# Optimization experiments

Measured on AMD Instinct MI355X. Metric: run time of the kernel, lower is better.

The kernel has to match this reference:

```python
import jax, jax.numpy as jnp
import numpy as np
from functools import partial

NP = 1024      # particles
T = 128        # timesteps
CUR_MIN, CUR_MAX = -2.0, 4.0
E_CRIT = 29000.0
F_STD = 0.005
G_STD = 0.01
NU = 1.0 / (G_STD * np.sqrt(2.0 * np.pi))

# VoC battery open-circuit-voltage curve constants
V_L, V_0 = -1.59614486, 4.13646328
GAMMA, ALPHA, BETA = 0.63726463, 1.40174122, 2.54478965


def voc(soc):
    return (V_L + (V_0 - V_L) * jnp.exp(GAMMA * (soc - 1.0))
            + ALPHA * V_L * (soc - 1.0)
            + (1.0 - ALPHA) * V_L * (jnp.exp(-BETA) - jnp.exp(-BETA * jnp.sqrt(soc))))


def setup_inputs() -> dict:
    key = jax.random.key(0)
    ks = jax.random.split(key, 11)
    soc_init = jax.random.uniform(ks[0], (NP, 1), jnp.float32, 0.3, 1.0)
    current = jax.random.normal(ks[1], (1, T), jnp.float32) * 0.5 + 1.0
    voltage_measured = 3.7 + 0.1 * jax.random.normal(ks[2], (1, T), jnp.float32)
    W1 = jax.random.normal(ks[3], (2, 1024), jnp.float32) / np.sqrt(2.0)
    b1 = jnp.zeros((1024,), jnp.float32)
    W2 = jax.random.normal(ks[4], (1024, 512), jnp.float32) / np.sqrt(1024.0)
    b2 = jnp.zeros((512,), jnp.float32)
    W3 = jax.random.normal(ks[5], (512, 1), jnp.float32) / np.sqrt(512.0)
    b3 = jnp.zeros((1,), jnp.float32)
    noise = jax.random.normal(ks[6], (T, NP, 1), jnp.float32)  # unit-std process noise
    u = jax.random.uniform(ks[7], (T,), jnp.float32)           # systematic-resampling offsets
    return {"soc_init": soc_init, "current": current, "voltage_measured": voltage_measured,
            "W1": W1, "b1": b1, "W2": W2, "b2": b2, "W3": W3, "b3": b3,
            "noise": noise, "u": u}


def _forward(soc_init, current, voltage_measured, W1, b1, W2, b2, W3, b3, noise, u):
    n = soc_init.shape[0]

    def mlp(x):  # [n,2] -> [n,1]
        z = jax.nn.sigmoid(x @ W1 + b1)
        z = jax.nn.sigmoid(z @ W2 + b2)
        return z @ W3 + b3

    def scale_I(I):
        return (I - CUR_MIN) / (CUR_MAX - CUR_MIN)

    cur = current[0]                       # [T]
    vmeas = voltage_measured[0]            # [T]
    cur_prev = jnp.concatenate([cur[:1], cur[:-1]])  # first step reuses current[0,0]

    def step(soc, xs):
        c_prev, c_t, vm, eps, ut = xs
        # --- prediction with previous current ---
        I = jnp.broadcast_to(c_prev, soc.shape)
        Z = mlp(jnp.concatenate([soc, scale_I(I)], axis=1))
        V = voc(soc) - I * Z
        soc = soc - I * V / E_CRIT + eps * F_STD
        soc = jnp.clip(soc, 1e-10, 1.0)
        # --- measurement update with current at t ---
        I = jnp.broadcast_to(c_t, soc.shape)
        sI = scale_I(I)
        Z = mlp(jnp.concatenate([soc, sI], axis=1))
        V = voc(soc) - I * Z
        logW = np.log(NU) - 0.5 * ((V - vm) / G_STD) ** 2  # [n,1]
        w = jnp.exp(logW - jnp.max(logW))[:, 0]
        wn = w / jnp.sum(w)
        # systematic resampling (deterministic given offset ut)
        cdf = jnp.cumsum(wn)
        pos = (ut + jnp.arange(n, dtype=jnp.float32)) / n
        idx = jnp.clip(jnp.searchsorted(cdf, pos), 0, n - 1)
        soc = soc[idx]
        # --- post-resample evaluation ---
        Z = mlp(jnp.concatenate([soc, sI], axis=1))
        V = voc(soc) - I * Z
        mse = jnp.mean((V - vm) ** 2)
        return soc, (mse, V[:, 0], soc[:, 0])

    soc0 = soc_init.astype(jnp.float32)
    _, (mses, Vs, socs) = jax.lax.scan(step, soc0, (cur_prev, cur, vmeas, noise, u))
    loss = jnp.mean(mses)        # == sum_t mse_t / T
    voltage = Vs.T               # [n, T]
    soc_hist = socs.T            # [n, T]
    return loss, voltage, soc_hist


def reference(soc_init, current, voltage_measured, W1, b1, W2, b2, W3, b3, noise, u):
    return _forward(soc_init, current, voltage_measured, W1, b1, W2, b2, W3, b3, noise, u)
```

## Files before the change

kernel.cpp:

```cpp
#include <hip/hip_runtime.h>
#include <stdint.h>

typedef __attribute__((ext_vector_type(8))) short short8;
typedef __attribute__((ext_vector_type(4))) float floatx4;

#define DONE_MAGIC 0x600DF00Du


__device__ __forceinline__ float sigm(float x) { return 1.0f / (1.0f + expf(-x)); }

__device__ __forceinline__ float vocf(float s) {
  const float V_L = -1.59614486f, V_0 = 4.13646328f;
  const float GAM = 0.63726463f, ALP = 1.40174122f, BET = 2.54478965f;
  return V_L + (V_0 - V_L) * expf(GAM * (s - 1.0f)) + ALP * V_L * (s - 1.0f)
       + (1.0f - ALP) * V_L * (expf(-BET) - expf(-BET * sqrtf(s)));
}

__device__ __forceinline__ unsigned short f2bf(float f) {
  unsigned u = __float_as_uint(f);
  u += 0x7FFFu + ((u >> 16) & 1u);
  return (unsigned short)(u >> 16);
}
__device__ __forceinline__ float bf2f(unsigned short b) {
  return __uint_as_float(((unsigned)b) << 16);
}

__device__ __forceinline__ float interp_c(const float* ctab, float s) {
  float f = s * 31.0f;
  float jf = fminf(floorf(f), 30.0f);
  int j = (int)jf;
  float u = f - jf;
  const float4 c = *(const float4*)&ctab[j * 4];
  return fmaf(fmaf(fmaf(c.w, u, c.z), u, c.y), u, c.x);
}

__device__ __forceinline__ int send_bl(float c, float u) {
  float C = c * 1024.0f;
  float sf = floorf(C - u);
  sf += (u + (sf + 1.0f) <= C) ? 1.0f : 0.0f;
  sf -= (u + sf > C) ? 1.0f : 0.0f;
  return (int)sf;
}

__device__ __forceinline__ float fast_exp2(float x) {
  float r;
  asm("v_exp_f32 %0, %1" : "=v"(r) : "v"(x));
  return r;
}


template<int C, int RM>
__device__ __forceinline__ float dpp_add_f(float x) {
  return __int_as_float(__builtin_amdgcn_update_dpp(0, __float_as_int(x), C, RM, 0xF, false));
}
template<int C, int RM>
__device__ __forceinline__ float dpp_old_f(float x) {
  return __int_as_float(__builtin_amdgcn_update_dpp(__float_as_int(x), __float_as_int(x), C, RM, 0xF, false));
}
template<int C, int RM>
__device__ __forceinline__ int dpp_old_i(int x) {
  return __builtin_amdgcn_update_dpp(x, x, C, RM, 0xF, false);
}
__device__ __forceinline__ float dpp_wshr1_f0(float x) {
  return __int_as_float(__builtin_amdgcn_update_dpp(0, __float_as_int(x), 0x138, 0xF, 0xF, true));
}
__device__ __forceinline__ int dpp_wshr1_i(int x, int old) {
  return __builtin_amdgcn_update_dpp(old, x, 0x138, 0xF, 0xF, false);
}
__device__ __forceinline__ int dpp_wshl1_i(int x, int old) {
  return __builtin_amdgcn_update_dpp(old, x, 0x130, 0xF, 0xF, false);
}

__device__ __forceinline__ float wave_iscan_add(float x) {
  x += dpp_add_f<0x111, 0xF>(x);
  x += dpp_add_f<0x112, 0xF>(x);
  x += dpp_add_f<0x114, 0xF>(x);
  x += dpp_add_f<0x118, 0xF>(x);
  x += dpp_add_f<0x142, 0xA>(x);
  x += dpp_add_f<0x143, 0xC>(x);
  return x;
}
__device__ __forceinline__ float wave_max_bcast(float x) {
  x = fmaxf(x, dpp_old_f<0xB1,  0xF>(x));
  x = fmaxf(x, dpp_old_f<0x4E,  0xF>(x));
  x = fmaxf(x, dpp_old_f<0x141, 0xF>(x));
  x = fmaxf(x, dpp_old_f<0x140, 0xF>(x));
  x = fmaxf(x, dpp_old_f<0x142, 0xA>(x));
  x = fmaxf(x, dpp_old_f<0x143, 0xC>(x));
  return __int_as_float(__builtin_amdgcn_readlane(__float_as_int(x), 63));
}
__device__ __forceinline__ int wave_iscan_max(int x) {
  x = max(x, dpp_old_i<0x111, 0xF>(x));
  x = max(x, dpp_old_i<0x112, 0xF>(x));
  x = max(x, dpp_old_i<0x114, 0xF>(x));
  x = max(x, dpp_old_i<0x118, 0xF>(x));
  x = max(x, dpp_old_i<0x142, 0xA>(x));
  x = max(x, dpp_old_i<0x143, 0xC>(x));
  return x;
}

__device__ __forceinline__ float rdlane_f(float x, int lane) {
  return __int_as_float(__builtin_amdgcn_readlane(__float_as_int(x), lane));
}

__device__ __forceinline__ void bar_lds() {
  asm volatile("s_waitcnt lgkmcnt(0)" ::: "memory");
  __builtin_amdgcn_s_barrier();
  asm volatile("" ::: "memory");
}


__global__ void __launch_bounds__(256)
k1_swizzle(const float* __restrict__ W2g, short* __restrict__ w2hiG, short* __restrict__ w2loG)
{
  int bid = blockIdx.x, tid = threadIdx.x;
  int pg = bid & 15, ng = bid >> 4;
  int u = pg * 256 + tid;
  int kb = u >> 7, l = u & 63, nt = (u >> 6) & 1, kq = l >> 4;
  int col = ng * 32 + nt * 16 + (l & 15);
  short8 hi8, lo8;
  #pragma unroll
  for (int j = 0; j < 8; j++) {
    int k = kb * 32 + kq * 8 + j;
    float w = W2g[k * 512 + col];
    unsigned short h = f2bf(w);
    hi8[j] = (short)h;
    lo8[j] = (short)f2bf(w - bf2f(h));
  }
  size_t off = ((size_t)ng * 4096 + u) * 8;
  *(short8*)(w2hiG + off) = hi8;
  *(short8*)(w2loG + off) = lo8;
}


__global__ void __launch_bounds__(256)
k2_gemm(const float* __restrict__ curg, const float* __restrict__ W1g,
        const float* __restrict__ b1g, const float* __restrict__ b2g,
        const float* __restrict__ W3g, const short* __restrict__ w2hiG,
        const short* __restrict__ w2loG, float* __restrict__ part)
{
  __shared__ short w2S[32768];
  __shared__ float b2S[32], w3S[32];

  const int tid = threadIdx.x, bid = blockIdx.x;
  const int ng = bid & 15, rtg = bid >> 4;
  const int wv = tid >> 6, ln = tid & 63;
  const int kq = ln >> 4;

  {
    const short* srcH = w2hiG + (size_t)ng * 32768;
    for (int i = tid; i < 4096; i += 256)
      *(short8*)(w2S + i * 8) = *(const short8*)(srcH + i * 8);
    if (tid < 32) { b2S[tid] = b2g[ng * 32 + tid]; w3S[tid] = W3g[ng * 32 + tid]; }
  }
  __syncthreads();

  const short* loG = w2loG + (size_t)ng * 32768;
  const int c = ln & 15, q = ln >> 4;
  const float b20 = b2S[c], b21 = b2S[16 + c];
  const float w30 = w3S[c], w31 = w3S[16 + c];

  for (int jj = 0; jj < 3; jj++) {
    int rt = rtg + 32 * jj;
    if (rt >= 72) break;
    int pt = rt * 4 + wv;
    unsigned r = pt * 16 + (ln & 15);
    unsigned t = r / 36u;
    int i = (int)(r - t * 36u);
    float soc = (float)(i - 1) * (1.0f / 31.0f);
    float sI = (curg[t] + 2.0f) / 6.0f;

    floatx4 acc0 = {0.f, 0.f, 0.f, 0.f};
    floatx4 acc1 = {0.f, 0.f, 0.f, 0.f};

    for (int kb = 0; kb < 32; kb++) {
      int k0 = kb * 32 + kq * 8;
      floatx4 wa0 = *(const floatx4*)(W1g + k0);
      floatx4 wa1 = *(const floatx4*)(W1g + k0 + 4);
      floatx4 wb0 = *(const floatx4*)(W1g + 1024 + k0);
      floatx4 wb1 = *(const floatx4*)(W1g + 1024 + k0 + 4);
      floatx4 bb0 = *(const floatx4*)(b1g + k0);
      floatx4 bb1 = *(const floatx4*)(b1g + k0 + 4);
      short8 ah, al;
      #pragma unroll
      for (int j = 0; j < 4; j++) {
        float x = soc * wa0[j] + sI * wb0[j] + bb0[j];
        float z = __builtin_amdgcn_rcpf(1.0f + __expf(-x));
        unsigned short h = f2bf(z);
        ah[j] = (short)h;
        al[j] = (short)f2bf(z - bf2f(h));
      }
      #pragma unroll
      for (int j = 0; j < 4; j++) {
        float x = soc * wa1[j] + sI * wb1[j] + bb1[j];
        float z = __builtin_amdgcn_rcpf(1.0f + __expf(-x));
        unsigned short h = f2bf(z);
        ah[4 + j] = (short)h;
        al[4 + j] = (short)f2bf(z - bf2f(h));
      }
      short8 bh0 = *(const short8*)(w2S + (kb * 2 + 0) * 512 + ln * 8);
      short8 bh1 = *(const short8*)(w2S + (kb * 2 + 1) * 512 + ln * 8);
      short8 bl0 = *(const short8*)(loG + (kb * 2 + 0) * 512 + ln * 8);
      short8 bl1 = *(const short8*)(loG + (kb * 2 + 1) * 512 + ln * 8);
      acc0 = __builtin_amdgcn_mfma_f32_16x16x32_bf16(ah, bh0, acc0, 0, 0, 0);
      acc1 = __builtin_amdgcn_mfma_f32_16x16x32_bf16(ah, bh1, acc1, 0, 0, 0);
      acc0 = __builtin_amdgcn_mfma_f32_16x16x32_bf16(ah, bl0, acc0, 0, 0, 0);
      acc1 = __builtin_amdgcn_mfma_f32_16x16x32_bf16(ah, bl1, acc1, 0, 0, 0);
      acc0 = __builtin_amdgcn_mfma_f32_16x16x32_bf16(al, bh0, acc0, 0, 0, 0);
      acc1 = __builtin_amdgcn_mfma_f32_16x16x32_bf16(al, bh1, acc1, 0, 0, 0);
    }

    #pragma unroll
    for (int r2 = 0; r2 < 4; r2++) {
      float v = w30 * sigm(acc0[r2] + b20) + w31 * sigm(acc1[r2] + b21);
      v += __shfl_xor(v, 1);
      v += __shfl_xor(v, 2);
      v += __shfl_xor(v, 4);
      v += __shfl_xor(v, 8);
      if (c == 0) part[(size_t)(pt * 16 + q * 4 + r2) * 16 + ng] = v;
    }
  }
}


__global__ void __launch_bounds__(256)
k3_table(const float* __restrict__ part, const float* __restrict__ b3g,
         const float* __restrict__ curg, float* __restrict__ VtabG)
{
  unsigned r = blockIdx.x * 256 + threadIdx.x;
  if (r < 4608) {
    const float* p = part + (size_t)r * 16;
    float s = 0.f;
    #pragma unroll
    for (int i = 0; i < 16; i++) s += p[i];
    float Z = s + b3g[0];
    unsigned t = r / 36u;
    int i = (int)(r - t * 36u);
    float node = (float)(i - 1) * (1.0f / 31.0f);
    float nodc = fmaxf(node, 1e-10f);
    VtabG[r] = vocf(nodc) - curg[t] * Z;
  }
}


__global__ void __launch_bounds__(256)
k3b_coeff(const float* __restrict__ VtabG, float* __restrict__ ctabG)
{
  int idx = blockIdx.x * 256 + threadIdx.x;
  if (idx < 3968) {
    int t = idx / 31, j = idx - t * 31;
    const float* nb = VtabG + t * 36 + j;
    float n0 = nb[0], n1 = nb[1], n2 = nb[2], n3 = nb[3];
    float c0 = n1;
    float c1 = (-2.0f * n0 - 3.0f * n1 + 6.0f * n2 - n3) * (1.0f / 6.0f);
    float c2 = (n0 - 2.0f * n1 + n2) * 0.5f;
    float c3 = (-n0 + 3.0f * (n1 - n2) + n3) * (1.0f / 6.0f);
    *(float4*)&ctabG[idx * 4] = make_float4(c0, c1, c2, c3);
  }
}


__device__ __forceinline__ int swzi(int j) { return ((j & 3) << 8) | (j >> 2); }

__global__ void __launch_bounds__(256)
pf_seq(const float* __restrict__ soc_init, const float* __restrict__ curg,
       const float* __restrict__ vmeasg, const float* __restrict__ noise_g,
       const float* __restrict__ u_g, const float* __restrict__ ctabG,
       float* __restrict__ vout, float* __restrict__ sout, float* __restrict__ outp,
       unsigned* __restrict__ flag)
{
  __shared__ float ctabS[15872];
  __shared__ float2 pvS[2][1024];
  __shared__ int   markS[1024] __attribute__((aligned(16)));
  __shared__ int   chunkS[4] __attribute__((aligned(16)));
  __shared__ float2 msS[4] __attribute__((aligned(16)));
  __shared__ float lossS[4];

  if (blockIdx.x != 0) {
    float a = 1.0000001f, b = 0.9999999f, c = 0.5f;
    while (__hip_atomic_load(flag, __ATOMIC_RELAXED, __HIP_MEMORY_SCOPE_AGENT) != DONE_MAGIC) {
      #pragma unroll 8
      for (int i = 0; i < 512; i++) { a = fmaf(a, c, b); b = fmaf(b, c, a); }
    }
    asm volatile("" :: "v"(a), "v"(b));
    return;
  }

  const int tid = threadIdx.x;
  const int w = tid >> 6, l = tid & 63;
  const int p0 = tid * 4;

  #pragma unroll
  for (int k = 0; k < 16; k++) {
    int i = tid + 256 * k;
    if (i < 3968) *(float4*)&ctabS[i * 4] = *(const float4*)&ctabG[i * 4];
  }
  float curA = curg[l],   curB = curg[64 + l];
  float vmA  = vmeasg[l], vmB  = vmeasg[64 + l];
  float uA   = u_g[l],    uB   = u_g[64 + l];
  *(int4*)&markS[p0] = make_int4(-1, -1, -1, -1);
  if (tid < 4) chunkS[tid] = -1;

  float sp0, sp1, sp2, sp3;
  {
    float4 s4 = *(const float4*)(soc_init + p0);
    float4 n4 = *(const float4*)(noise_g + p0);
    bar_lds();
    float c0 = rdlane_f(curA, 0);
    float c02 = c0 * (1.0f / 29000.0f);
    float spv[4];
    #pragma unroll
    for (int r = 0; r < 4; r++) {
      float si = ((const float*)&s4)[r];
      float V0 = interp_c(ctabS, si);
      float spn = fmaf(((const float*)&n4)[r], 0.005f, fmaf(-c02, V0, si));
      spv[r] = __builtin_amdgcn_fmed3f(spn, 1e-10f, 1.0f);
    }
    sp0 = spv[0]; sp1 = spv[1]; sp2 = spv[2]; sp3 = spv[3];
  }

  float lossAcc = 0.0f;

  for (int t = 0; t < 128; t++) {
    const float* ctab = ctabS + t * 124;
    const int cb = t & 1;
    float cI, vm, ut;
    if (t < 64) { cI = rdlane_f(curA, t); vm = rdlane_f(vmA, t); ut = rdlane_f(uA, t); }
    else        { cI = rdlane_f(curB, t - 64); vm = rdlane_f(vmB, t - 64); ut = rdlane_f(uB, t - 64); }
    float cI2 = cI * (1.0f / 29000.0f);

    int tn = (t < 127) ? t + 1 : 127;
    float4 noi4 = *(const float4*)(noise_g + tn * 1024 + p0);

    float V10 = interp_c(ctab, sp0);
    float V11 = interp_c(ctab, sp1);
    float V12 = interp_c(ctab, sp2);
    float V13 = interp_c(ctab, sp3);
    pvS[cb][tid]       = make_float2(sp0, V10);
    pvS[cb][256 + tid] = make_float2(sp1, V11);
    pvS[cb][512 + tid] = make_float2(sp2, V12);
    pvS[cb][768 + tid] = make_float2(sp3, V13);
    float d0 = V10 - vm, d1 = V11 - vm, d2 = V12 - vm, d3 = V13 - vm;
    float lw0 = d0 * d0 * -7213.4755594f;
    float lw1 = d1 * d1 * -7213.4755594f;
    float lw2 = d2 * d2 * -7213.4755594f;
    float lw3 = d3 * d3 * -7213.4755594f;

    float lmax = fmaxf(fmaxf(lw0, lw1), fmaxf(lw2, lw3));
    float mw = wave_max_bcast(lmax);
    float pr0, pr1, pr2, pr3, acc;
    {
      float w0 = fast_exp2(lw0 - mw); acc = w0;    pr0 = acc;
      float w1 = fast_exp2(lw1 - mw); acc += w1;   pr1 = acc;
      float w2 = fast_exp2(lw2 - mw); acc += w2;   pr2 = acc;
      float w3 = fast_exp2(lw3 - mw); acc += w3;   pr3 = acc;
    }
    float isc = wave_iscan_add(acc);
    if (l == 63) msS[w] = make_float2(mw, isc);
    bar_lds();

    float4 ms01 = *(const float4*)&msS[0];
    float4 ms23 = *(const float4*)&msS[2];
    float m = fmaxf(fmaxf(ms01.x, ms01.z), fmaxf(ms23.x, ms23.z));
    float f0 = fast_exp2(ms01.x - m), f1 = fast_exp2(ms01.z - m);
    float f2 = fast_exp2(ms23.x - m), f3 = fast_exp2(ms23.w == ms23.w ? ms23.z - m : 0.f);
    f3 = fast_exp2(ms23.z - m);
    float t0 = ms01.y * f0, t1 = ms01.w * f1, t2 = ms23.y * f2, t3 = ms23.w * f3;
    float total = (t0 + t1) + (t2 + t3);
    float woff = (w > 0 ? t0 : 0.0f) + (w > 1 ? t1 : 0.0f) + (w > 2 ? t2 : 0.0f);
    float fw = (w == 0) ? f0 : ((w == 1) ? f1 : ((w == 2) ? f2 : f3));
    float exclw = dpp_wshr1_f0(isc);
    float rS = 1.0f / total;

    int se0 = send_bl(fmaf(exclw + pr0, fw, woff) * rS, ut);
    int se1 = send_bl(fmaf(exclw + pr1, fw, woff) * rS, ut);
    int se2 = send_bl(fmaf(exclw + pr2, fw, woff) * rS, ut);
    int se3 = send_bl(fmaf(exclw + pr3, fw, woff) * rS, ut);

    int nxt = dpp_wshl1_i(se0, se3);
    int tbase = t << 10;
    if (tid == 0 && se0 >= 0) { markS[0] = tbase; atomicMax(&chunkS[0], tbase); }
    if (se1 > se0 && se0 < 1023) {
      int s = se0 + 1, tg = tbase | (p0 + 1);
      markS[swzi(s)] = tg; atomicMax(&chunkS[s >> 8], tg);
    }
    if (se2 > se1 && se1 < 1023) {
      int s = se1 + 1, tg = tbase | (p0 + 2);
      markS[swzi(s)] = tg; atomicMax(&chunkS[s >> 8], tg);
    }
    if (se3 > se2 && se2 < 1023) {
      int s = se2 + 1, tg = tbase | (p0 + 3);
      markS[swzi(s)] = tg; atomicMax(&chunkS[s >> 8], tg);
    }
    if (l != 63) {
      if (nxt > se3 && se3 < 1023) {
        int s = se3 + 1, tg = tbase | (p0 + 4);
        markS[swzi(s)] = tg; atomicMax(&chunkS[s >> 8], tg);
      }
    } else {
      if (se3 < 1023) {
        int s = se3 + 1;
        int tg = (tid == 255) ? (tbase | 1023) : (tbase | (p0 + 4));
        atomicMax(&markS[swzi(s)], tg); atomicMax(&chunkS[s >> 8], tg);
      }
    }
    bar_lds();

    int mk0 = markS[tid],       mk1 = markS[256 + tid];
    int mk2 = markS[512 + tid], mk3 = markS[768 + tid];
    int4 ch4 = *(const int4*)chunkS;
    int q0 = mk0;
    int q1 = max(q0, mk1);
    int q2 = max(q1, mk2);
    int q3 = max(q2, mk3);
    int iscI = wave_iscan_max(q3);
    int ex = dpp_wshr1_i(iscI, -1);
    if (w > 0) ex = max(ex, ch4.x);
    if (w > 1) ex = max(ex, ch4.y);
    if (w > 2) ex = max(ex, ch4.z);

    int o0 = max(ex, q0) & 1023, o1 = max(ex, q1) & 1023;
    int o2 = max(ex, q2) & 1023, o3 = max(ex, q3) & 1023;
    float2 g0 = pvS[cb][swzi(o0)];
    float2 g1 = pvS[cb][swzi(o1)];
    float2 g2 = pvS[cb][swzi(o2)];
    float2 g3 = pvS[cb][swzi(o3)];

    *(float4*)(vout + t * 1024 + p0) = make_float4(g0.y, g1.y, g2.y, g3.y);
    *(float4*)(sout + t * 1024 + p0) = make_float4(g0.x, g1.x, g2.x, g3.x);

    float e0 = g0.y - vm, e1 = g1.y - vm, e2 = g2.y - vm, e3 = g3.y - vm;
    lossAcc = fmaf(e0, e0, lossAcc);
    lossAcc = fmaf(e1, e1, lossAcc);
    lossAcc = fmaf(e2, e2, lossAcc);
    lossAcc = fmaf(e3, e3, lossAcc);
    const float* nz = (const float*)&noi4;
    sp0 = __builtin_amdgcn_fmed3f(fmaf(nz[0], 0.005f, fmaf(-cI2, g0.y, g0.x)), 1e-10f, 1.0f);
    sp1 = __builtin_amdgcn_fmed3f(fmaf(nz[1], 0.005f, fmaf(-cI2, g1.y, g1.x)), 1e-10f, 1.0f);
    sp2 = __builtin_amdgcn_fmed3f(fmaf(nz[2], 0.005f, fmaf(-cI2, g2.y, g2.x)), 1e-10f, 1.0f);
    sp3 = __builtin_amdgcn_fmed3f(fmaf(nz[3], 0.005f, fmaf(-cI2, g3.y, g3.x)), 1e-10f, 1.0f);
  }

  float ls = wave_iscan_add(lossAcc);
  if (l == 63) lossS[w] = ls;
  bar_lds();
  if (tid == 0) {
    outp[0] = (lossS[0] + lossS[1] + lossS[2] + lossS[3]) * (1.0f / 131072.0f);
    __hip_atomic_store(flag, DONE_MAGIC, __ATOMIC_RELEASE, __HIP_MEMORY_SCOPE_AGENT);
  }
}


__global__ void __launch_bounds__(256)
k5_transpose(const float* __restrict__ vout, const float* __restrict__ sout,
             float* __restrict__ outp)
{
  __shared__ float tile[128 * 65];
  const int bid = blockIdx.x;
  const int arr = bid & 1;
  const int pg = bid >> 1;
  const float* src = arr ? sout : vout;
  float* dst = outp + 1 + arr * 131072;
  const int tid = threadIdx.x;
  const int p0 = pg * 64;

  #pragma unroll 4
  for (int s = 0; s < 32; s++) {
    int t = s * 4 + (tid >> 6);
    int p = tid & 63;
    tile[t * 65 + p] = src[t * 1024 + p0 + p];
  }
  __syncthreads();
  #pragma unroll 4
  for (int s = 0; s < 32; s++) {
    int pl = s * 2 + (tid >> 7);
    int t = tid & 127;
    dst[(p0 + pl) * 128 + t] = tile[t * 65 + pl];
  }
}


extern "C" void kernel_launch(void* const* d_in, const int* in_sizes, int n_in,
                              void* d_out, int out_size, void* d_ws, size_t ws_size,
                              hipStream_t stream) {
  const float* soc_init = (const float*)d_in[0];
  const float* cur      = (const float*)d_in[1];
  const float* vmeas    = (const float*)d_in[2];
  const float* W1       = (const float*)d_in[3];
  const float* b1       = (const float*)d_in[4];
  const float* W2       = (const float*)d_in[5];
  const float* b2       = (const float*)d_in[6];
  const float* W3       = (const float*)d_in[7];
  const float* b3       = (const float*)d_in[8];
  const float* noise    = (const float*)d_in[9];
  const float* u        = (const float*)d_in[10];
  float* out = (float*)d_out;
  char* ws = (char*)d_ws;

  short* w2hi   = (short*)ws;
  short* w2lo   = (short*)(ws + (1 << 20));
  float* part   = (float*)(ws + (2 << 20));
  char*  p3     = ws + (2 << 20) + 4608 * 16 * 4;
  float* VtabG  = (float*)p3;
  float* ctabG  = (float*)(p3 + 4608 * 4);
  float* vout   = (float*)(p3 + 4608 * 4 + 3968 * 16);
  float* sout   = (float*)(p3 + 4608 * 4 + 3968 * 16 + 1024 * 128 * 4);
  unsigned* flag = (unsigned*)(p3 + 4608 * 4 + 3968 * 16 + 2 * 1024 * 128 * 4);

  k1_swizzle<<<256, 256, 0, stream>>>(W2, w2hi, w2lo);
  k2_gemm<<<512, 256, 0, stream>>>(cur, W1, b1, b2, W3, w2hi, w2lo, part);
  k3_table<<<18, 256, 0, stream>>>(part, b3, cur, VtabG);
  k3b_coeff<<<16, 256, 0, stream>>>(VtabG, ctabG);
  pf_seq<<<256, 256, 0, stream>>>(soc_init, cur, vmeas, noise, u, ctabG, vout, sout, out, flag);
  k5_transpose<<<32, 256, 0, stream>>>(vout, sout, out);
}
```

Before: 332.4 us.

## Run sequential particle-filter block with 512 threads, two particles per thread

Result: no change. 338.3 us (+1.8%).

```diff
diff --git a/kernel.cpp b/kernel.cpp
--- a/kernel.cpp
+++ b/kernel.cpp
@@ -260,9 +260,9 @@
 }
 
 
-__device__ __forceinline__ int swzi(int j) { return ((j & 3) << 8) | (j >> 2); }
-
-__global__ void __launch_bounds__(256)
+__device__ __forceinline__ int swzi(int j) { return ((j & 1) << 9) | (j >> 1); }
+
+__global__ void __launch_bounds__(512)
 pf_seq(const float* __restrict__ soc_init, const float* __restrict__ curg,
        const float* __restrict__ vmeasg, const float* __restrict__ noise_g,
        const float* __restrict__ u_g, const float* __restrict__ ctabG,
@@ -272,9 +272,9 @@
   __shared__ float ctabS[15872];
   __shared__ float2 pvS[2][1024];
   __shared__ int   markS[1024] __attribute__((aligned(16)));
-  __shared__ int   chunkS[4] __attribute__((aligned(16)));
-  __shared__ float2 msS[4] __attribute__((aligned(16)));
-  __shared__ float lossS[4];
+  __shared__ int   chunkS[8] __attribute__((aligned(16)));
+  __shared__ float2 msS[8] __attribute__((aligned(16)));
+  __shared__ float lossS[8];
 
   if (blockIdx.x != 0) {
     float a = 1.0000001f, b = 0.9999999f, c = 0.5f;
@@ -288,35 +288,30 @@
 
   const int tid = threadIdx.x;
   const int w = tid >> 6, l = tid & 63;
-  const int p0 = tid * 4;
+  const int p0 = tid * 2;
 
   #pragma unroll
-  for (int k = 0; k < 16; k++) {
-    int i = tid + 256 * k;
+  for (int k = 0; k < 8; k++) {
+    int i = tid + 512 * k;
     if (i < 3968) *(float4*)&ctabS[i * 4] = *(const float4*)&ctabG[i * 4];
   }
   float curA = curg[l],   curB = curg[64 + l];
   float vmA  = vmeasg[l], vmB  = vmeasg[64 + l];
   float uA   = u_g[l],    uB   = u_g[64 + l];
-  *(int4*)&markS[p0] = make_int4(-1, -1, -1, -1);
-  if (tid < 4) chunkS[tid] = -1;
-
-  float sp0, sp1, sp2, sp3;
+  *(int2*)&markS[p0] = make_int2(-1, -1);
+  if (tid < 8) chunkS[tid] = -1;
+
+  float sp0, sp1;
   {
-    float4 s4 = *(const float4*)(soc_init + p0);
-    float4 n4 = *(const float4*)(noise_g + p0);
+    float2 s2 = *(const float2*)(soc_init + p0);
+    float2 n2 = *(const float2*)(noise_g + p0);
     bar_lds();
     float c0 = rdlane_f(curA, 0);
     float c02 = c0 * (1.0f / 29000.0f);
-    float spv[4];
-    #pragma unroll
-    for (int r = 0; r < 4; r++) {
-      float si = ((const float*)&s4)[r];
-      float V0 = interp_c(ctabS, si);
-      float spn = fmaf(((const float*)&n4)[r], 0.005f, fmaf(-c02, V0, si));
-      spv[r] = __builtin_amdgcn_fmed3f(spn, 1e-10f, 1.0f);
-    }
-    sp0 = spv[0]; sp1 = spv[1]; sp2 = spv[2]; sp3 = spv[3];
+    float V00 = interp_c(ctabS, s2.x);
+    float V01 = interp_c(ctabS, s2.y);
+    sp0 = __builtin_amdgcn_fmed3f(fmaf(n2.x, 0.005f, fmaf(-c02, V00, s2.x)), 1e-10f, 1.0f);
+    sp1 = __builtin_amdgcn_fmed3f(fmaf(n2.y, 0.005f, fmaf(-c02, V01, s2.y)), 1e-10f, 1.0f);
   }
 
   float lossAcc = 0.0f;
@@ -330,122 +325,107 @@
     float cI2 = cI * (1.0f / 29000.0f);
 
     int tn = (t < 127) ? t + 1 : 127;
-    float4 noi4 = *(const float4*)(noise_g + tn * 1024 + p0);
+    float2 noi2 = *(const float2*)(noise_g + tn * 1024 + p0);
 
     float V10 = interp_c(ctab, sp0);
     float V11 = interp_c(ctab, sp1);
-    float V12 = interp_c(ctab, sp2);
-    float V13 = interp_c(ctab, sp3);
     pvS[cb][tid]       = make_float2(sp0, V10);
-    pvS[cb][256 + tid] = make_float2(sp1, V11);
-    pvS[cb][512 + tid] = make_float2(sp2, V12);
-    pvS[cb][768 + tid] = make_float2(sp3, V13);
-    float d0 = V10 - vm, d1 = V11 - vm, d2 = V12 - vm, d3 = V13 - vm;
+    pvS[cb][512 + tid] = make_float2(sp1, V11);
+    float d0 = V10 - vm, d1 = V11 - vm;
     float lw0 = d0 * d0 * -7213.4755594f;
     float lw1 = d1 * d1 * -7213.4755594f;
-    float lw2 = d2 * d2 * -7213.4755594f;
-    float lw3 = d3 * d3 * -7213.4755594f;
-
-    float lmax = fmaxf(fmaxf(lw0, lw1), fmaxf(lw2, lw3));
-    float mw = wave_max_bcast(lmax);
-    float pr0, pr1, pr2, pr3, acc;
+
+    float mw = wave_max_bcast(fmaxf(lw0, lw1));
+    float pr0, pr1, acc;
     {
       float w0 = fast_exp2(lw0 - mw); acc = w0;    pr0 = acc;
       float w1 = fast_exp2(lw1 - mw); acc += w1;   pr1 = acc;
-      float w2 = fast_exp2(lw2 - mw); acc += w2;   pr2 = acc;
-      float w3 = fast_exp2(lw3 - mw); acc += w3;   pr3 = acc;
     }
     float isc = wave_iscan_add(acc);
     if (l == 63) msS[w] = make_float2(mw, isc);
     bar_lds();
 
-    float4 ms01 = *(const float4*)&msS[0];
-    float4 ms23 = *(const float4*)&msS[2];
-    float m = fmaxf(fmaxf(ms01.x, ms01.z), fmaxf(ms23.x, ms23.z));
-    float f0 = fast_exp2(ms01.x - m), f1 = fast_exp2(ms01.z - m);
-    float f2 = fast_exp2(ms23.x - m), f3 = fast_exp2(ms23.w == ms23.w ? ms23.z - m : 0.f);
-    f3 = fast_exp2(ms23.z - m);
-    float t0 = ms01.y * f0, t1 = ms01.w * f1, t2 = ms23.y * f2, t3 = ms23.w * f3;
-    float total = (t0 + t1) + (t2 + t3);
-    float woff = (w > 0 ? t0 : 0.0f) + (w > 1 ? t1 : 0.0f) + (w > 2 ? t2 : 0.0f);
-    float fw = (w == 0) ? f0 : ((w == 1) ? f1 : ((w == 2) ? f2 : f3));
+    float4 msA = *(const float4*)&msS[0];
+    float4 msB = *(const float4*)&msS[2];
+    float4 msC = *(const float4*)&msS[4];
+    float4 msD = *(const float4*)&msS[6];
+    float m = fmaxf(fmaxf(fmaxf(msA.x, msA.z), fmaxf(msB.x, msB.z)),
+                    fmaxf(fmaxf(msC.x, msC.z), fmaxf(msD.x, msD.z)));
+    float f0 = fast_exp2(msA.x - m), f1 = fast_exp2(msA.z - m);
+    float f2 = fast_exp2(msB.x - m), f3 = fast_exp2(msB.z - m);
+    float f4 = fast_exp2(msC.x - m), f5 = fast_exp2(msC.z - m);
+    float f6 = fast_exp2(msD.x - m), f7 = fast_exp2(msD.z - m);
+    float t0 = msA.y * f0, t1 = msA.w * f1, t2 = msB.y * f2, t3 = msB.w * f3;
+    float t4 = msC.y * f4, t5 = msC.w * f5, t6 = msD.y * f6, t7 = msD.w * f7;
+    float total = ((t0 + t1) + (t2 + t3)) + ((t4 + t5) + (t6 + t7));
+    float woff = (w > 0 ? t0 : 0.0f) + (w > 1 ? t1 : 0.0f) + (w > 2 ? t2 : 0.0f)
+               + (w > 3 ? t3 : 0.0f) + (w > 4 ? t4 : 0.0f) + (w > 5 ? t5 : 0.0f)
+               + (w > 6 ? t6 : 0.0f);
+    float fw = (w == 0) ? f0 : ((w == 1) ? f1 : ((w == 2) ? f2 : ((w == 3) ? f3 :
+               ((w == 4) ? f4 : ((w == 5) ? f5 : ((w == 6) ? f6 : f7))))));
     float exclw = dpp_wshr1_f0(isc);
     float rS = 1.0f / total;
 
     int se0 = send_bl(fmaf(exclw + pr0, fw, woff) * rS, ut);
     int se1 = send_bl(fmaf(exclw + pr1, fw, woff) * rS, ut);
-    int se2 = send_bl(fmaf(exclw + pr2, fw, woff) * rS, ut);
-    int se3 = send_bl(fmaf(exclw + pr3, fw, woff) * rS, ut);
-
-    int nxt = dpp_wshl1_i(se0, se3);
+
+    int nxt = dpp_wshl1_i(se0, se1);
     int tbase = t << 10;
     if (tid == 0 && se0 >= 0) { markS[0] = tbase; atomicMax(&chunkS[0], tbase); }
     if (se1 > se0 && se0 < 1023) {
       int s = se0 + 1, tg = tbase | (p0 + 1);
-      markS[swzi(s)] = tg; atomicMax(&chunkS[s >> 8], tg);
-    }
-    if (se2 > se1 && se1 < 1023) {
-      int s = se1 + 1, tg = tbase | (p0 + 2);
-      markS[swzi(s)] = tg; atomicMax(&chunkS[s >> 8], tg);
-    }
-    if (se3 > se2 && se2 < 1023) {
-      int s = se2 + 1, tg = tbase | (p0 + 3);
-      markS[swzi(s)] = tg; atomicMax(&chunkS[s >> 8], tg);
+      markS[swzi(s)] = tg; atomicMax(&chunkS[s >> 7], tg);
     }
     if (l != 63) {
-      if (nxt > se3 && se3 < 1023) {
-        int s = se3 + 1, tg = tbase | (p0 + 4);
-        markS[swzi(s)] = tg; atomicMax(&chunkS[s >> 8], tg);
+      if (nxt > se1 && se1 < 1023) {
+        int s = se1 + 1, tg = tbase | (p0 + 2);
+        markS[swzi(s)] = tg; atomicMax(&chunkS[s >> 7], tg);
       }
     } else {
-      if (se3 < 1023) {
-        int s = se3 + 1;
-        int tg = (tid == 255) ? (tbase | 1023) : (tbase | (p0 + 4));
-        atomicMax(&markS[swzi(s)], tg); atomicMax(&chunkS[s >> 8], tg);
+      if (se1 < 1023) {
+        int s = se1 + 1;
+        int tg = (tid == 511) ? (tbase | 1023) : (tbase | (p0 + 2));
+        atomicMax(&markS[swzi(s)], tg); atomicMax(&chunkS[s >> 7], tg);
       }
     }
     bar_lds();
 
-    int mk0 = markS[tid],       mk1 = markS[256 + tid];
-    int mk2 = markS[512 + tid], mk3 = markS[768 + tid];
-    int4 ch4 = *(const int4*)chunkS;
+    int mk0 = markS[tid], mk1 = markS[512 + tid];
+    int4 chA = *(const int4*)&chunkS[0];
+    int4 chB = *(const int4*)&chunkS[4];
     int q0 = mk0;
     int q1 = max(q0, mk1);
-    int q2 = max(q1, mk2);
-    int q3 = max(q2, mk3);
-    int iscI = wave_iscan_max(q3);
+    int iscI = wave_iscan_max(q1);
     int ex = dpp_wshr1_i(iscI, -1);
-    if (w > 0) ex = max(ex, ch4.x);
-    if (w > 1) ex = max(ex, ch4.y);
-    if (w > 2) ex = max(ex, ch4.z);
+    if (w > 0) ex = max(ex, chA.x);
+    if (w > 1) ex = max(ex, chA.y);
+    if (w > 2) ex = max(ex, chA.z);
+    if (w > 3) ex = max(ex, chA.w);
+    if (w > 4) ex = max(ex, chB.x);
+    if (w > 5) ex = max(ex, chB.y);
+    if (w > 6) ex = max(ex, chB.z);
 
     int o0 = max(ex, q0) & 1023, o1 = max(ex, q1) & 1023;
-    int o2 = max(ex, q2) & 1023, o3 = max(ex, q3) & 1023;
     float2 g0 = pvS[cb][swzi(o0)];
     float2 g1 = pvS[cb][swzi(o1)];
-    float2 g2 = pvS[cb][swzi(o2)];
-    float2 g3 = pvS[cb][swzi(o3)];
-
-    *(float4*)(vout + t * 1024 + p0) = make_float4(g0.y, g1.y, g2.y, g3.y);
-    *(float4*)(sout + t * 1024 + p0) = make_float4(g0.x, g1.x, g2.x, g3.x);
-
-    float e0 = g0.y - vm, e1 = g1.y - vm, e2 = g2.y - vm, e3 = g3.y - vm;
+
+    *(float2*)(vout + t * 1024 + p0) = make_float2(g0.y, g1.y);
+    *(float2*)(sout + t * 1024 + p0) = make_float2(g0.x, g1.x);
+
+    float e0 = g0.y - vm, e1 = g1.y - vm;
     lossAcc = fmaf(e0, e0, lossAcc);
     lossAcc = fmaf(e1, e1, lossAcc);
-    lossAcc = fmaf(e2, e2, lossAcc);
-    lossAcc = fmaf(e3, e3, lossAcc);
-    const float* nz = (const float*)&noi4;
-    sp0 = __builtin_amdgcn_fmed3f(fmaf(nz[0], 0.005f, fmaf(-cI2, g0.y, g0.x)), 1e-10f, 1.0f);
-    sp1 = __builtin_amdgcn_fmed3f(fmaf(nz[1], 0.005f, fmaf(-cI2, g1.y, g1.x)), 1e-10f, 1.0f);
-    sp2 = __builtin_amdgcn_fmed3f(fmaf(nz[2], 0.005f, fmaf(-cI2, g2.y, g2.x)), 1e-10f, 1.0f);
-    sp3 = __builtin_amdgcn_fmed3f(fmaf(nz[3], 0.005f, fmaf(-cI2, g3.y, g3.x)), 1e-10f, 1.0f);
+    sp0 = __builtin_amdgcn_fmed3f(fmaf(noi2.x, 0.005f, fmaf(-cI2, g0.y, g0.x)), 1e-10f, 1.0f);
+    sp1 = __builtin_amdgcn_fmed3f(fmaf(noi2.y, 0.005f, fmaf(-cI2, g1.y, g1.x)), 1e-10f, 1.0f);
   }
 
   float ls = wave_iscan_add(lossAcc);
   if (l == 63) lossS[w] = ls;
   bar_lds();
   if (tid == 0) {
-    outp[0] = (lossS[0] + lossS[1] + lossS[2] + lossS[3]) * (1.0f / 131072.0f);
+    float s = ((lossS[0] + lossS[1]) + (lossS[2] + lossS[3]))
+            + ((lossS[4] + lossS[5]) + (lossS[6] + lossS[7]));
+    outp[0] = s * (1.0f / 131072.0f);
     __hip_atomic_store(flag, DONE_MAGIC, __ATOMIC_RELEASE, __HIP_MEMORY_SCOPE_AGENT);
   }
 }
@@ -511,6 +491,6 @@
   k2_gemm<<<512, 256, 0, stream>>>(cur, W1, b1, b2, W3, w2hi, w2lo, part);
   k3_table<<<18, 256, 0, stream>>>(part, b3, cur, VtabG);
   k3b_coeff<<<16, 256, 0, stream>>>(VtabG, ctabG);
-  pf_seq<<<256, 256, 0, stream>>>(soc_init, cur, vmeas, noise, u, ctabG, vout, sout, out, flag);
+  pf_seq<<<256, 512, 0, stream>>>(soc_init, cur, vmeas, noise, u, ctabG, vout, sout, out, flag);
   k5_transpose<<<32, 256, 0, stream>>>(vout, sout, out);
 }
```
